# Optimization experiments

Measured on AMD Instinct MI355X. Metric: run time of the kernel, lower is better.

The kernel has to match this reference:

```python
import jax, jax.numpy as jnp
import numpy as np

S, B, D = 2048, 32, 1024  # seq_len, batch, in_dim; out_dim = 2*D

def setup_inputs() -> dict:
    key = jax.random.key(0)
    k1, k2, k3, k4 = jax.random.split(key, 4)
    return {
        "input": jax.random.normal(k1, (S, B, D), dtype=jnp.float32),
        "h": jax.random.normal(k2, (B, D), dtype=jnp.float32),
        "Wi": jax.random.normal(k3, (D, D), dtype=jnp.float32) * 0.02,
        "Wo": jax.random.normal(k4, (D, 2 * D), dtype=jnp.float32) * 0.02,
    }

def reference(input, h, Wi, Wo):
    # semi = Wi(h), broadcast over seq dim (torch expand_as)
    semi = h @ Wi.T                                   # [B, D]
    # score logits: elementwise mult + sum over feature dim
    logits = jnp.einsum('sbd,bd->bs', input, semi)    # [B, S]
    # legacy nn.Softmax() on 2D tensor normalizes over dim=1 (= seq)
    attn = jax.nn.softmax(logits, axis=1)             # [B, S]
    # weighted sum over sequence
    s_tilde = jnp.einsum('bs,sbd->bd', attn, input)   # [B, D]
    # output projection + tanh
    c_t = jnp.tanh(jnp.concatenate([s_tilde, h], axis=1) @ Wo.T)  # [B, D]
    return c_t
```

## Files before the change

kernel.cpp:

```cpp
#include <hip/hip_runtime.h>
#include <math.h>

#define S_LEN    2048
#define BATCH    32
#define DIM      1024
#define P_CHUNKS 32
#define CHUNK    (S_LEN / P_CHUNKS)
#define ROWS_PER_WAVE (CHUNK / 4)

__global__ __launch_bounds__(256) void gemm_skinny(
    const float* __restrict__ A, const float* __restrict__ W,
    float* __restrict__ out, int K, int Dout, int act)
{
    __shared__ __align__(16) float At[2][32 * 256];

    const int t    = threadIdx.x;
    const int lane = t & 63;
    const int wid  = t >> 6;
    const int d    = blockIdx.x * 4 + wid;

    float acc[32];
#pragma unroll
    for (int b = 0; b < 32; ++b) acc[b] = 0.0f;

    float4 sreg[8];
#pragma unroll
    for (int i = 0; i < 8; ++i) {
        int f4id = t + i * 256;
        int bb   = f4id >> 6;
        int c4   = f4id & 63;
        sreg[i] = ((const float4*)(A + (size_t)bb * K))[c4];
    }
    float4 w4 = ((const float4*)(W + (size_t)d * K))[lane];

    int buf = 0;
    for (int k0 = 0; k0 < K; k0 += 256) {
#pragma unroll
        for (int i = 0; i < 8; ++i) {
            int f4id = t + i * 256;
            int bb   = f4id >> 6;
            int c4   = f4id & 63;
            ((float4*)At[buf])[bb * 64 + c4] = sreg[i];
        }
        __syncthreads();

        float4 w4c = w4;
        if (k0 + 256 < K) {
            const int k1 = k0 + 256;
#pragma unroll
            for (int i = 0; i < 8; ++i) {
                int f4id = t + i * 256;
                int bb   = f4id >> 6;
                int c4   = f4id & 63;
                sreg[i] = ((const float4*)(A + (size_t)bb * K + k1))[c4];
            }
            w4 = ((const float4*)(W + (size_t)d * K + k1))[lane];
        }

#pragma unroll
        for (int b = 0; b < 32; ++b) {
            float4 a4 = ((const float4*)At[buf])[b * 64 + lane];
            acc[b] = fmaf(w4c.x, a4.x, acc[b]);
            acc[b] = fmaf(w4c.y, a4.y, acc[b]);
            acc[b] = fmaf(w4c.z, a4.z, acc[b]);
            acc[b] = fmaf(w4c.w, a4.w, acc[b]);
        }
        buf ^= 1;
    }

    float mine = 0.0f;
#pragma unroll
    for (int b = 0; b < 32; ++b) {
        float v = acc[b];
#pragma unroll
        for (int off = 32; off > 0; off >>= 1) v += __shfl_xor(v, off, 64);
        if (lane == b) mine = v;
    }
    if (lane < 32) {
        float o = act ? tanhf(mine) : mine;
        out[(size_t)lane * Dout + d] = o;
    }
}

__global__ __launch_bounds__(256) void attn_partial(
    const float* __restrict__ input, const float* __restrict__ semi,
    float* __restrict__ pacc, float* __restrict__ pm, float* __restrict__ pl)
{
    const int p    = blockIdx.x;
    const int b    = blockIdx.y;
    const int t    = threadIdx.x;
    const int lane = t & 63;
    const int w    = t >> 6;
    const int s0   = p * CHUNK + w * ROWS_PER_WAVE;

    __shared__ __align__(16) float accs[4][DIM];
    __shared__ float smw[4], slw[4];

    const float4* sp = (const float4*)(semi + (size_t)b * DIM);
    const float4 sm0 = sp[lane];
    const float4 sm1 = sp[lane + 64];
    const float4 sm2 = sp[lane + 128];
    const float4 sm3 = sp[lane + 192];

    const float4* rp = (const float4*)(input + ((size_t)s0 * BATCH + b) * DIM);
    const size_t rstride = (size_t)BATCH * DIM / 4;

    float m = -INFINITY, l = 0.0f;
    float4 a0 = make_float4(0.f, 0.f, 0.f, 0.f);
    float4 a1 = a0, a2 = a0, a3 = a0;

    float4 x0 = rp[lane], x1 = rp[lane + 64], x2 = rp[lane + 128], x3 = rp[lane + 192];

#pragma unroll 1
    for (int j = 0; j < ROWS_PER_WAVE; ++j) {
        const float4 c0 = x0, c1 = x1, c2 = x2, c3 = x3;
        if (j + 1 < ROWS_PER_WAVE) {
            const float4* np = rp + (size_t)(j + 1) * rstride;
            x0 = np[lane];       x1 = np[lane + 64];
            x2 = np[lane + 128]; x3 = np[lane + 192];
        }

        float pd = c0.x * sm0.x;
        pd = fmaf(c0.y, sm0.y, pd); pd = fmaf(c0.z, sm0.z, pd); pd = fmaf(c0.w, sm0.w, pd);
        pd = fmaf(c1.x, sm1.x, pd); pd = fmaf(c1.y, sm1.y, pd);
        pd = fmaf(c1.z, sm1.z, pd); pd = fmaf(c1.w, sm1.w, pd);
        pd = fmaf(c2.x, sm2.x, pd); pd = fmaf(c2.y, sm2.y, pd);
        pd = fmaf(c2.z, sm2.z, pd); pd = fmaf(c2.w, sm2.w, pd);
        pd = fmaf(c3.x, sm3.x, pd); pd = fmaf(c3.y, sm3.y, pd);
        pd = fmaf(c3.w, sm3.w, pd); pd = fmaf(c3.z, sm3.z, pd);

#pragma unroll
        for (int off = 32; off > 0; off >>= 1) pd += __shfl_xor(pd, off, 64);

        if (pd > m + 8.0f) {
            const float sc = __expf(m - pd);
            a0.x *= sc; a0.y *= sc; a0.z *= sc; a0.w *= sc;
            a1.x *= sc; a1.y *= sc; a1.z *= sc; a1.w *= sc;
            a2.x *= sc; a2.y *= sc; a2.z *= sc; a2.w *= sc;
            a3.x *= sc; a3.y *= sc; a3.z *= sc; a3.w *= sc;
            l *= sc;
            m = pd;
        }
        const float f = __expf(pd - m);
        a0.x = fmaf(f, c0.x, a0.x); a0.y = fmaf(f, c0.y, a0.y);
        a0.z = fmaf(f, c0.z, a0.z); a0.w = fmaf(f, c0.w, a0.w);
        a1.x = fmaf(f, c1.x, a1.x); a1.y = fmaf(f, c1.y, a1.y);
        a1.z = fmaf(f, c1.z, a1.z); a1.w = fmaf(f, c1.w, a1.w);
        a2.x = fmaf(f, c2.x, a2.x); a2.y = fmaf(f, c2.y, a2.y);
        a2.z = fmaf(f, c2.z, a2.z); a2.w = fmaf(f, c2.w, a2.w);
        a3.x = fmaf(f, c3.x, a3.x); a3.y = fmaf(f, c3.y, a3.y);
        a3.z = fmaf(f, c3.z, a3.z); a3.w = fmaf(f, c3.w, a3.w);
        l += f;
    }

    float4* as = (float4*)accs[w];
    as[lane]       = a0;
    as[lane + 64]  = a1;
    as[lane + 128] = a2;
    as[lane + 192] = a3;
    if (lane == 0) { smw[w] = m; slw[w] = l; }
    __syncthreads();

    const float M  = fmaxf(fmaxf(smw[0], smw[1]), fmaxf(smw[2], smw[3]));
    const float f0 = __expf(smw[0] - M);
    const float f1 = __expf(smw[1] - M);
    const float f2 = __expf(smw[2] - M);
    const float f3 = __expf(smw[3] - M);

    const float4 r0 = ((const float4*)accs[0])[t];
    const float4 r1 = ((const float4*)accs[1])[t];
    const float4 r2 = ((const float4*)accs[2])[t];
    const float4 r3 = ((const float4*)accs[3])[t];
    float4 o;
    o.x = fmaf(f3, r3.x, fmaf(f2, r2.x, fmaf(f1, r1.x, f0 * r0.x)));
    o.y = fmaf(f3, r3.y, fmaf(f2, r2.y, fmaf(f1, r1.y, f0 * r0.y)));
    o.z = fmaf(f3, r3.z, fmaf(f2, r2.z, fmaf(f1, r1.z, f0 * r0.z)));
    o.w = fmaf(f3, r3.w, fmaf(f2, r2.w, fmaf(f1, r1.w, f0 * r0.w)));

    ((float4*)(pacc + ((size_t)b * P_CHUNKS + p) * DIM))[t] = o;
    if (t == 0) {
        pm[b * P_CHUNKS + p] = M;
        pl[b * P_CHUNKS + p] =
            fmaf(f3, slw[3], fmaf(f2, slw[2], fmaf(f1, slw[1], f0 * slw[0])));
    }
}

__global__ __launch_bounds__(256) void combine(
    const float* __restrict__ pacc, const float* __restrict__ pm,
    const float* __restrict__ pl, const float* __restrict__ h,
    float* __restrict__ cat)
{
    const int b = blockIdx.x;
    const int q = blockIdx.y;
    const int t = threadIdx.x;

    __shared__ float fsc[P_CHUNKS];
    __shared__ float Linv;

    if (t < 32) {
        const float mv = pm[b * P_CHUNKS + t];
        const float lv = pl[b * P_CHUNKS + t];
        float mx = mv;
#pragma unroll
        for (int off = 16; off > 0; off >>= 1)
            mx = fmaxf(mx, __shfl_xor(mx, off, 64));
        const float f = __expf(mv - mx);
        fsc[t] = f;
        float L = lv * f;
#pragma unroll
        for (int off = 16; off > 0; off >>= 1) L += __shfl_xor(L, off, 64);
        if (t == 0) Linv = 1.0f / L;
    }
    __syncthreads();

    const int d = q * 256 + t;
    const float* pb = pacc + (size_t)b * P_CHUNKS * DIM + d;
    float s0 = 0.f, s1 = 0.f, s2 = 0.f, s3 = 0.f;
#pragma unroll
    for (int pp = 0; pp < P_CHUNKS; pp += 4) {
        s0 = fmaf(fsc[pp + 0], pb[(size_t)(pp + 0) * DIM], s0);
        s1 = fmaf(fsc[pp + 1], pb[(size_t)(pp + 1) * DIM], s1);
        s2 = fmaf(fsc[pp + 2], pb[(size_t)(pp + 2) * DIM], s2);
        s3 = fmaf(fsc[pp + 3], pb[(size_t)(pp + 3) * DIM], s3);
    }
    const float sum = (s0 + s1) + (s2 + s3);

    cat[(size_t)b * (2 * DIM) + d]       = sum * Linv;
    cat[(size_t)b * (2 * DIM) + DIM + d] = h[(size_t)b * DIM + d];
}

extern "C" void kernel_launch(void* const* d_in, const int* in_sizes, int n_in,
                              void* d_out, int out_size, void* d_ws, size_t ws_size,
                              hipStream_t stream)
{
    const float* input = (const float*)d_in[0];
    const float* h     = (const float*)d_in[1];
    const float* Wi    = (const float*)d_in[2];
    const float* Wo    = (const float*)d_in[3];
    float* out = (float*)d_out;

    float* ws   = (float*)d_ws;
    float* semi = ws;
    float* pacc = semi + 32 * 1024;
    float* pm   = pacc + (size_t)32 * P_CHUNKS * 1024;
    float* pl   = pm + 32 * P_CHUNKS;
    float* cat  = pl + 32 * P_CHUNKS;

    hipLaunchKernelGGL(gemm_skinny, dim3(256), dim3(256), 0, stream,
                       h, Wi, semi, 1024, 1024, 0);
    hipLaunchKernelGGL(attn_partial, dim3(P_CHUNKS, BATCH), dim3(256), 0, stream,
                       input, semi, pacc, pm, pl);
    hipLaunchKernelGGL(combine, dim3(BATCH, 4), dim3(256), 0, stream,
                       pacc, pm, pl, h, cat);
    hipLaunchKernelGGL(gemm_skinny, dim3(256), dim3(256), 0, stream,
                       cat, Wo, out, 2048, 1024, 1);
}
```

Before: 413.8 us.

## Fuse split-softmax combine into attn_partial via last-block atomic counter

Removes the separate combine kernel launch. Each batch row keeps an atomic counter, zeroed by the first gemm launch, and the last of the 32 chunk blocks to finish does the cross-chunk softmax merge using float4 loads and writes the concat buffer. Launch bounds on attn_partial also gain a min-blocks hint of 4. This saves one launch and its gap, but the merge now runs in only 32 blocks and every block pays a fence and an atomic.

```diff
diff --git a/kernel.cpp b/kernel.cpp
--- a/kernel.cpp
+++ b/kernel.cpp
@@ -10,7 +10,8 @@
 
 __global__ __launch_bounds__(256) void gemm_skinny(
     const float* __restrict__ A, const float* __restrict__ W,
-    float* __restrict__ out, int K, int Dout, int act)
+    float* __restrict__ out, int K, int Dout, int act,
+    unsigned* __restrict__ cnt)
 {
     __shared__ __align__(16) float At[2][32 * 256];
 
@@ -18,6 +19,8 @@
     const int lane = t & 63;
     const int wid  = t >> 6;
     const int d    = blockIdx.x * 4 + wid;
+
+    if (cnt && blockIdx.x == 0 && t < BATCH) cnt[t] = 0u;
 
     float acc[32];
 #pragma unroll
@@ -82,9 +85,11 @@
     }
 }
 
-__global__ __launch_bounds__(256) void attn_partial(
+__global__ __launch_bounds__(256, 4) void attn_partial(
     const float* __restrict__ input, const float* __restrict__ semi,
-    float* __restrict__ pacc, float* __restrict__ pm, float* __restrict__ pl)
+    float* __restrict__ pacc, float* __restrict__ pm, float* __restrict__ pl,
+    const float* __restrict__ h, float* __restrict__ cat,
+    unsigned* __restrict__ cnt)
 {
     const int p    = blockIdx.x;
     const int b    = blockIdx.y;
@@ -95,6 +100,9 @@
 
     __shared__ __align__(16) float accs[4][DIM];
     __shared__ float smw[4], slw[4];
+    __shared__ unsigned is_last;
+    __shared__ float fsc[P_CHUNKS];
+    __shared__ float Linv;
 
     const float4* sp = (const float4*)(semi + (size_t)b * DIM);
     const float4 sm0 = sp[lane];
@@ -127,7 +135,7 @@
         pd = fmaf(c2.x, sm2.x, pd); pd = fmaf(c2.y, sm2.y, pd);
         pd = fmaf(c2.z, sm2.z, pd); pd = fmaf(c2.w, sm2.w, pd);
         pd = fmaf(c3.x, sm3.x, pd); pd = fmaf(c3.y, sm3.y, pd);
-        pd = fmaf(c3.w, sm3.w, pd); pd = fmaf(c3.z, sm3.z, pd);
+        pd = fmaf(c3.z, sm3.z, pd); pd = fmaf(c3.w, sm3.w, pd);
 
 #pragma unroll
         for (int off = 32; off > 0; off >>= 1) pd += __shfl_xor(pd, off, 64);
@@ -183,50 +191,62 @@
         pl[b * P_CHUNKS + p] =
             fmaf(f3, slw[3], fmaf(f2, slw[2], fmaf(f1, slw[1], f0 * slw[0])));
     }
-}
-
-__global__ __launch_bounds__(256) void combine(
-    const float* __restrict__ pacc, const float* __restrict__ pm,
-    const float* __restrict__ pl, const float* __restrict__ h,
-    float* __restrict__ cat)
-{
-    const int b = blockIdx.x;
-    const int q = blockIdx.y;
-    const int t = threadIdx.x;
-
-    __shared__ float fsc[P_CHUNKS];
-    __shared__ float Linv;
-
-    if (t < 32) {
+
+    __threadfence();
+    __syncthreads();
+    if (t == 0) {
+        unsigned old = __hip_atomic_fetch_add(&cnt[b], 1u,
+                         __ATOMIC_ACQ_REL, __HIP_MEMORY_SCOPE_AGENT);
+        is_last = (old == P_CHUNKS - 1) ? 1u : 0u;
+    }
+    __syncthreads();
+    if (!is_last) return;
+
+    if (t < P_CHUNKS) {
         const float mv = pm[b * P_CHUNKS + t];
         const float lv = pl[b * P_CHUNKS + t];
         float mx = mv;
 #pragma unroll
         for (int off = 16; off > 0; off >>= 1)
             mx = fmaxf(mx, __shfl_xor(mx, off, 64));
-        const float f = __expf(mv - mx);
-        fsc[t] = f;
-        float L = lv * f;
+        const float fsv = __expf(mv - mx);
+        fsc[t] = fsv;
+        float L = lv * fsv;
 #pragma unroll
         for (int off = 16; off > 0; off >>= 1) L += __shfl_xor(L, off, 64);
         if (t == 0) Linv = 1.0f / L;
     }
     __syncthreads();
 
-    const int d = q * 256 + t;
-    const float* pb = pacc + (size_t)b * P_CHUNKS * DIM + d;
-    float s0 = 0.f, s1 = 0.f, s2 = 0.f, s3 = 0.f;
+    const float4* pb4 = (const float4*)(pacc + (size_t)b * P_CHUNKS * DIM);
+    float4 s0v = make_float4(0.f, 0.f, 0.f, 0.f);
+    float4 s1v = s0v, s2v = s0v, s3v = s0v;
 #pragma unroll
     for (int pp = 0; pp < P_CHUNKS; pp += 4) {
-        s0 = fmaf(fsc[pp + 0], pb[(size_t)(pp + 0) * DIM], s0);
-        s1 = fmaf(fsc[pp + 1], pb[(size_t)(pp + 1) * DIM], s1);
-        s2 = fmaf(fsc[pp + 2], pb[(size_t)(pp + 2) * DIM], s2);
-        s3 = fmaf(fsc[pp + 3], pb[(size_t)(pp + 3) * DIM], s3);
-    }
-    const float sum = (s0 + s1) + (s2 + s3);
-
-    cat[(size_t)b * (2 * DIM) + d]       = sum * Linv;
-    cat[(size_t)b * (2 * DIM) + DIM + d] = h[(size_t)b * DIM + d];
+        const float4 v0 = pb4[(size_t)(pp + 0) * (DIM / 4) + t];
+        const float4 v1 = pb4[(size_t)(pp + 1) * (DIM / 4) + t];
+        const float4 v2 = pb4[(size_t)(pp + 2) * (DIM / 4) + t];
+        const float4 v3 = pb4[(size_t)(pp + 3) * (DIM / 4) + t];
+        const float g0 = fsc[pp + 0], g1 = fsc[pp + 1];
+        const float g2 = fsc[pp + 2], g3 = fsc[pp + 3];
+        s0v.x = fmaf(g0, v0.x, s0v.x); s0v.y = fmaf(g0, v0.y, s0v.y);
+        s0v.z = fmaf(g0, v0.z, s0v.z); s0v.w = fmaf(g0, v0.w, s0v.w);
+        s1v.x = fmaf(g1, v1.x, s1v.x); s1v.y = fmaf(g1, v1.y, s1v.y);
+        s1v.z = fmaf(g1, v1.z, s1v.z); s1v.w = fmaf(g1, v1.w, s1v.w);
+        s2v.x = fmaf(g2, v2.x, s2v.x); s2v.y = fmaf(g2, v2.y, s2v.y);
+        s2v.z = fmaf(g2, v2.z, s2v.z); s2v.w = fmaf(g2, v2.w, s2v.w);
+        s3v.x = fmaf(g3, v3.x, s3v.x); s3v.y = fmaf(g3, v3.y, s3v.y);
+        s3v.z = fmaf(g3, v3.z, s3v.z); s3v.w = fmaf(g3, v3.w, s3v.w);
+    }
+    float4 sum;
+    sum.x = ((s0v.x + s1v.x) + (s2v.x + s3v.x)) * Linv;
+    sum.y = ((s0v.y + s1v.y) + (s2v.y + s3v.y)) * Linv;
+    sum.z = ((s0v.z + s1v.z) + (s2v.z + s3v.z)) * Linv;
+    sum.w = ((s0v.w + s1v.w) + (s2v.w + s3v.w)) * Linv;
+
+    float4* cat4 = (float4*)(cat + (size_t)b * (2 * DIM));
+    cat4[t]             = sum;
+    cat4[DIM / 4 + t]   = ((const float4*)(h + (size_t)b * DIM))[t];
 }
 
 extern "C" void kernel_launch(void* const* d_in, const int* in_sizes, int n_in,
@@ -245,13 +265,12 @@
     float* pm   = pacc + (size_t)32 * P_CHUNKS * 1024;
     float* pl   = pm + 32 * P_CHUNKS;
     float* cat  = pl + 32 * P_CHUNKS;
+    unsigned* cnt = (unsigned*)(cat + 32 * 2 * DIM);
 
     hipLaunchKernelGGL(gemm_skinny, dim3(256), dim3(256), 0, stream,
-                       h, Wi, semi, 1024, 1024, 0);
+                       h, Wi, semi, 1024, 1024, 0, cnt);
     hipLaunchKernelGGL(attn_partial, dim3(P_CHUNKS, BATCH), dim3(256), 0, stream,
-                       input, semi, pacc, pm, pl);
-    hipLaunchKernelGGL(combine, dim3(BATCH, 4), dim3(256), 0, stream,
-                       pacc, pm, pl, h, cat);
+                       input, semi, pacc, pm, pl, h, cat, cnt);
     hipLaunchKernelGGL(gemm_skinny, dim3(256), dim3(256), 0, stream,
-                       cat, Wo, out, 2048, 1024, 1);
+                       cat, Wo, out, 2048, 1024, 1, (unsigned*)nullptr);
 }
```

Measured after the change: 585.0 us. 41.4% more time.
